# Kernel optimization log

Measured on AMD Instinct MI355X. Metric: run time of the kernel, lower is better.

The kernel has to match this reference:

```python
import jax, jax.numpy as jnp
import numpy as np

N_NODES = 100000
N_EDGES = 1600000
D = 64
N_LAYERS = 5  # hops=4 -> hops+1 GraphConv layers


def setup_inputs() -> dict:
    key = jax.random.key(0)
    k1, k2, k3, k4, k5, k6 = jax.random.split(key, 6)
    x = jax.random.normal(k1, (N_NODES, D), dtype=jnp.float32)
    edge_index = jax.random.randint(k2, (2, N_EDGES), 0, N_NODES, dtype=jnp.int64)
    edge_weight = jax.random.uniform(k3, (N_EDGES,), dtype=jnp.float32)
    # Per-layer params (all dims are 64 so we can stack): PyG GraphConv has
    # lin_rel (with bias) applied to the aggregated messages and lin_root
    # (no bias) applied to the node's own features.
    scale = 1.0 / np.sqrt(D)
    W_rel = jax.random.normal(k4, (N_LAYERS, D, D), dtype=jnp.float32) * scale
    b_rel = jnp.zeros((N_LAYERS, D), dtype=jnp.float32)
    W_root = jax.random.normal(k5, (N_LAYERS, D, D), dtype=jnp.float32) * scale
    return {"x": x, "edge_index": edge_index, "edge_weight": edge_weight,
            "W_rel": W_rel, "b_rel": b_rel, "W_root": W_root}


def _graph_conv(x, src, dst, edge_weight, W_rel_i, b_rel_i, W_root_i):
    # message: x_j * w_e ; aggregate: scatter-add onto destination nodes
    msg = x[src] * edge_weight[:, None]               # [E, D] gather
    agg = jax.ops.segment_sum(msg, dst, num_segments=N_NODES)  # [N, D] scatter
    return agg @ W_rel_i + b_rel_i + x @ W_root_i


def reference(x, edge_index, edge_weight, W_rel, b_rel, W_root):
    src, dst = edge_index[0], edge_index[1]
    h = x
    for i in range(N_LAYERS - 1):
        h = _graph_conv(h, src, dst, edge_weight, W_rel[i], b_rel[i], W_root[i])
        h = jax.nn.relu(h)
    h = _graph_conv(h, src, dst, edge_weight, W_rel[-1], b_rel[-1], W_root[-1])
    return h
```

## Files before the change

### kernel.cpp

```cpp
#include <hip/hip_runtime.h>

#define N_NODES 100000
#define N_EDGES 1600000
#define D 64
#define N_LAYERS 5
#define FB 1000
#define BN 100
#define NX 8
#define BCAP_X 320
#define BCAP 2048
#define BIN_BLOCKS 512
#define BIN_THREADS 512
#define BIN_CHUNK 3125

typedef unsigned short u16;
typedef unsigned long long u64;
typedef __attribute__((ext_vector_type(8))) short bf16x8;
typedef __attribute__((ext_vector_type(4))) float f32x4;

__device__ __forceinline__ float bf2f(u16 u) {
    union { unsigned int i; float f; } v;
    v.i = ((unsigned int)u) << 16;
    return v.f;
}
__device__ __forceinline__ u16 f2bf(float f) {
    union { float f; unsigned int i; } v;
    v.f = f;
    unsigned int r = v.i + 0x7FFFu + ((v.i >> 16) & 1u);
    return (u16)(r >> 16);
}
__device__ __forceinline__ float bf2f_lo(unsigned int pk) {
    union { unsigned int i; float f; } v;
    v.i = pk << 16;
    return v.f;
}
__device__ __forceinline__ float bf2f_hi(unsigned int pk) {
    union { unsigned int i; float f; } v;
    v.i = pk & 0xFFFF0000u;
    return v.f;
}


__global__ __launch_bounds__(1024) void initcur_kernel(int* __restrict__ fcur)
{
    int i = blockIdx.x * 1024 + threadIdx.x;
    if (i < NX * FB) fcur[i] = i * BCAP_X;
}

__global__ __launch_bounds__(BIN_THREADS) void bin_kernel(
    const int* __restrict__ src, const int* __restrict__ dst,
    const float* __restrict__ ew, int* __restrict__ fcur,
    u64* __restrict__ stag)
{
    __shared__ int hc[FB];
    const int xbase = (blockIdx.x & (NX - 1)) * FB;
    for (int b = threadIdx.x; b < FB; b += BIN_THREADS) hc[b] = 0;
    __syncthreads();
    const int e0 = blockIdx.x * BIN_CHUNK;
    for (int e = e0 + threadIdx.x; e < e0 + BIN_CHUNK; e += BIN_THREADS) {
        int d = dst[e];
        atomicAdd(&hc[d / BN], 1);
    }
    __syncthreads();
    for (int b = threadIdx.x; b < FB; b += BIN_THREADS) {
        int c = hc[b];
        if (c) hc[b] = atomicAdd(&fcur[xbase + b], c);
    }
    __syncthreads();
    for (int e = e0 + threadIdx.x; e < e0 + BIN_CHUNK; e += BIN_THREADS) {
        int d = dst[e];
        int b = d / BN;
        int pos = atomicAdd(&hc[b], 1);
        int s   = __builtin_nontemporal_load(&src[e]);
        float w = __builtin_nontemporal_load(&ew[e]);
        unsigned int pk = (unsigned int)((d - b * BN) << 17) | (unsigned int)s;
        u64 rec = ((u64)(unsigned int)__float_as_int(w) << 32) | pk;
        stag[pos] = rec;
    }
}

__global__ __launch_bounds__(1024) void fscan_kernel(
    const int* __restrict__ fcur, int* __restrict__ fbase,
    int* __restrict__ rowptr)
{
    __shared__ int s[1024];
    int t = threadIdx.x;
    int v = 0;
    if (t < FB) {
        #pragma unroll
        for (int x = 0; x < NX; ++x) {
            int cell = x * FB + t;
            v += fcur[cell] - cell * BCAP_X;
        }
    }
    s[t] = v;
    __syncthreads();
    for (int off = 1; off < 1024; off <<= 1) {
        int u = (t >= off) ? s[t - off] : 0;
        __syncthreads();
        s[t] += u;
        __syncthreads();
    }
    if (t < FB) fbase[t] = s[t] - v;
    if (t == FB - 1) {
        fbase[FB] = s[t];
        rowptr[N_NODES] = s[t];
    }
}

__global__ __launch_bounds__(256) void sort_kernel(
    const u64* __restrict__ stag, const int* __restrict__ fcur,
    const int* __restrict__ fbase, int* __restrict__ rowptr,
    int2* __restrict__ edges)
{
    __shared__ u64 ls[BCAP];
    __shared__ int cnt[BN];
    __shared__ int cur[BN];
    __shared__ int sc[128];
    const int b = blockIdx.x;
    const int base = fbase[b];
    const int t = threadIdx.x;
    for (int i = t; i < BN; i += 256) cnt[i] = 0;
    __syncthreads();
    int ofs = 0;
    #pragma unroll
    for (int x = 0; x < NX; ++x) {
        int cell = x * FB + b;
        int sz = fcur[cell] - cell * BCAP_X;
        const u64* sp = stag + (size_t)cell * BCAP_X;
        for (int i = t; i < sz; i += 256) {
            u64 r = __builtin_nontemporal_load(&sp[i]);
            ls[ofs + i] = r;
            atomicAdd(&cnt[((unsigned int)r) >> 17], 1);
        }
        ofs += sz;
    }
    const int size = ofs;
    __syncthreads();
    if (t < 128) sc[t] = (t < BN) ? cnt[t] : 0;
    __syncthreads();
    for (int off = 1; off < 128; off <<= 1) {
        int u = 0;
        if (t < 128 && t >= off) u = sc[t - off];
        __syncthreads();
        if (t < 128) sc[t] += u;
        __syncthreads();
    }
    if (t < BN) {
        int excl = sc[t] - cnt[t];
        rowptr[b * BN + t] = base + excl;
        cur[t] = excl;
    }
    __syncthreads();
    for (int i = t; i < size; i += 256) {
        u64 r = ls[i];
        unsigned int lo = (unsigned int)r;
        int dloc = lo >> 17;
        int rank = atomicAdd(&cur[dloc], 1);
        edges[base + rank] = make_int2((int)(lo & 0x1FFFFu),
                                       (int)(unsigned int)(r >> 32));
    }
}

__global__ __launch_bounds__(256) void f2bf_kernel(
    const float* __restrict__ in, u16* __restrict__ out)
{
    int i = blockIdx.x * 256 + threadIdx.x;
    if (i >= (N_NODES * D) / 4) return;
    float4 v = ((const float4*)in)[i];
    ushort4 o;
    o.x = f2bf(v.x); o.y = f2bf(v.y); o.z = f2bf(v.z); o.w = f2bf(v.w);
    ((ushort4*)out)[i] = o;
}

__global__ __launch_bounds__(256) void wprep_kernel(
    const float* __restrict__ Wrel, const float* __restrict__ Wroot,
    u16* __restrict__ W2T)
{
    int i = blockIdx.x * 256 + threadIdx.x;
    if (i >= N_LAYERS * 64 * 128) return;
    int l = i / (64 * 128);
    int rem = i % (64 * 128);
    int n = rem >> 7;
    int k = rem & 127;
    float v = (k < 64) ? Wrel[l * 4096 + k * 64 + n]
                       : Wroot[l * 4096 + (k - 64) * 64 + n];
    W2T[i] = f2bf(v);
}

__global__ __launch_bounds__(512) void layer_kernel(
    const u16* __restrict__ hin, const int* __restrict__ rowptr,
    const int2* __restrict__ edges, const u16* __restrict__ W2T,
    const float* __restrict__ brel,
    u16* __restrict__ hout_bf, float* __restrict__ hout_f32, int relu)
{
    __shared__ u16 aggs[16][64];
    const int wave = threadIdx.x >> 6;
    const int lane = threadIdx.x & 63;
    const int nb16 = blockIdx.x * 16;
    const int sl   = lane & 31;
    const int half = lane >> 5;

    {
        int nl = 2 * wave + half;
        int node = nb16 + nl;
        float acc0 = 0.f, acc1 = 0.f;
        int b = rowptr[node];
        int e = rowptr[node + 1];
        for (int base = b; base < e; base += 32) {
            int cnt = min(32, e - base);
            int idx = 0;
            float wv = 0.f;
            if (sl < cnt) {
                int2 p = edges[base + sl];
                idx = p.x;
                wv = __int_as_float(p.y);
            }
            int j = 0;
            for (; j + 8 <= cnt; j += 8) {
                int s0 = __shfl(idx, j + 0, 32), s1 = __shfl(idx, j + 1, 32);
                int s2 = __shfl(idx, j + 2, 32), s3 = __shfl(idx, j + 3, 32);
                int s4 = __shfl(idx, j + 4, 32), s5 = __shfl(idx, j + 5, 32);
                int s6 = __shfl(idx, j + 6, 32), s7 = __shfl(idx, j + 7, 32);
                float w0 = __shfl(wv, j + 0, 32), w1 = __shfl(wv, j + 1, 32);
                float w2 = __shfl(wv, j + 2, 32), w3 = __shfl(wv, j + 3, 32);
                float w4 = __shfl(wv, j + 4, 32), w5 = __shfl(wv, j + 5, 32);
                float w6 = __shfl(wv, j + 6, 32), w7 = __shfl(wv, j + 7, 32);
                unsigned int p0 = *(const unsigned int*)(hin + ((size_t)s0 << 6) + sl * 2);
                unsigned int p1 = *(const unsigned int*)(hin + ((size_t)s1 << 6) + sl * 2);
                unsigned int p2 = *(const unsigned int*)(hin + ((size_t)s2 << 6) + sl * 2);
                unsigned int p3 = *(const unsigned int*)(hin + ((size_t)s3 << 6) + sl * 2);
                unsigned int p4 = *(const unsigned int*)(hin + ((size_t)s4 << 6) + sl * 2);
                unsigned int p5 = *(const unsigned int*)(hin + ((size_t)s5 << 6) + sl * 2);
                unsigned int p6 = *(const unsigned int*)(hin + ((size_t)s6 << 6) + sl * 2);
                unsigned int p7 = *(const unsigned int*)(hin + ((size_t)s7 << 6) + sl * 2);
                acc0 += bf2f_lo(p0) * w0 + bf2f_lo(p1) * w1
                      + bf2f_lo(p2) * w2 + bf2f_lo(p3) * w3
                      + bf2f_lo(p4) * w4 + bf2f_lo(p5) * w5
                      + bf2f_lo(p6) * w6 + bf2f_lo(p7) * w7;
                acc1 += bf2f_hi(p0) * w0 + bf2f_hi(p1) * w1
                      + bf2f_hi(p2) * w2 + bf2f_hi(p3) * w3
                      + bf2f_hi(p4) * w4 + bf2f_hi(p5) * w5
                      + bf2f_hi(p6) * w6 + bf2f_hi(p7) * w7;
            }
            for (; j < cnt; ++j) {
                int s = __shfl(idx, j, 32);
                float w = __shfl(wv, j, 32);
                unsigned int pk = *(const unsigned int*)(hin + ((size_t)s << 6) + sl * 2);
                acc0 += bf2f_lo(pk) * w;
                acc1 += bf2f_hi(pk) * w;
            }
        }
        int u16idx = (nl << 6) | ((sl * 2) ^ ((nl & 7) << 3));
        unsigned int o = ((unsigned int)f2bf(acc1) << 16) | f2bf(acc0);
        *(unsigned int*)(&aggs[0][0] + u16idx) = o;
    }
    __syncthreads();

    if (wave < 4) {
        const int nt = wave;
        const int m = lane & 15;
        const int q = lane >> 4;

        bf16x8 a[4];
        {
            int r0 = (m << 6) | ((q * 8) ^ ((m & 7) << 3));
            int r1 = (m << 6) | ((32 + q * 8) ^ ((m & 7) << 3));
            a[0] = *(const bf16x8*)(&aggs[0][0] + r0);
            a[1] = *(const bf16x8*)(&aggs[0][0] + r1);
        }
        size_t rowa = (size_t)(nb16 + m) << 6;
        a[2] = *(const bf16x8*)(hin + rowa + q * 8);
        a[3] = *(const bf16x8*)(hin + rowa + 32 + q * 8);

        bf16x8 bfr[4];
        #pragma unroll
        for (int kk = 0; kk < 4; ++kk)
            bfr[kk] = *(const bf16x8*)(W2T + (size_t)(nt * 16 + m) * 128
                                       + kk * 32 + q * 8);

        float bv = brel[nt * 16 + m];
        f32x4 acc = (f32x4){bv, bv, bv, bv};
        #pragma unroll
        for (int kk = 0; kk < 4; ++kk)
            acc = __builtin_amdgcn_mfma_f32_16x16x32_bf16(a[kk], bfr[kk],
                                                          acc, 0, 0, 0);

        #pragma unroll
        for (int r = 0; r < 4; ++r) {
            int n2 = nb16 + q * 4 + r;
            float v = acc[r];
            if (relu) v = fmaxf(v, 0.f);
            int dim = nt * 16 + m;
            if (hout_f32) hout_f32[(size_t)n2 * 64 + dim] = v;
            else          hout_bf [(size_t)n2 * 64 + dim] = f2bf(v);
        }
    }
}

extern "C" void kernel_launch(void* const* d_in, const int* in_sizes, int n_in,
                              void* d_out, int out_size, void* d_ws, size_t ws_size,
                              hipStream_t stream)
{
    const float* x     = (const float*)d_in[0];
    const int*   ei    = (const int*)d_in[1];
    const float* ew    = (const float*)d_in[2];
    const float* Wrel  = (const float*)d_in[3];
    const float* brel  = (const float*)d_in[4];
    const float* Wroot = (const float*)d_in[5];
    float* out = (float*)d_out;

    const int* src = ei;
    const int* dst = ei + N_EDGES;

    const size_t featb_bytes = (size_t)N_NODES * D * 2;
    char* ws = (char*)d_ws;
    size_t off = 0;
    u16*  hb     = (u16*)(ws + off);  off += featb_bytes;
    u16*  hb2    = (u16*)(ws + off);  off += featb_bytes;
    u16*  W2T    = (u16*)(ws + off);  off += (size_t)N_LAYERS * 64 * 128 * 2;
    int*  rowptr = (int*)(ws + off);  off += 400016;
    int*  fcur   = (int*)(ws + off);  off += NX * FB * 4;
    int*  fbase  = (int*)(ws + off);  off += (FB + 1) * 4 + 60;
    int2* edges  = (int2*)(ws + off); off += (size_t)N_EDGES * 8;

    u64* stag = (u64*)ws;

    u16* hbuf[2] = {hb, hb2};

    const int cblocks = (N_NODES * D / 4 + 255) / 256;
    const int wblocks = (N_LAYERS * 64 * 128 + 255) / 256;
    const int lblocks = N_NODES / 16;

    initcur_kernel<<<8, 1024, 0, stream>>>(fcur);
    bin_kernel<<<BIN_BLOCKS, BIN_THREADS, 0, stream>>>(src, dst, ew, fcur, stag);
    fscan_kernel<<<1, 1024, 0, stream>>>(fcur, fbase, rowptr);
    sort_kernel<<<FB, 256, 0, stream>>>(stag, fcur, fbase, rowptr, edges);
    f2bf_kernel<<<cblocks, 256, 0, stream>>>(x, hb);
    wprep_kernel<<<wblocks, 256, 0, stream>>>(Wrel, Wroot, W2T);

    for (int layer = 0; layer < N_LAYERS; ++layer) {
        int last = (layer == N_LAYERS - 1);
        layer_kernel<<<lblocks, 512, 0, stream>>>(
            hbuf[layer & 1], rowptr, edges,
            W2T + (size_t)layer * 64 * 128,
            brel + (size_t)layer * D,
            last ? nullptr : hbuf[(layer + 1) & 1],
            last ? out : nullptr,
            last ? 0 : 1);
    }
}
```

Baseline: 397.2 us.

## Assign one wave per node with half-waves splitting edges, scalar edge loads

The gather phase changes from two nodes per wave (each half-wave handling one node) to one node per wave, with the two half-waves processing alternate edges and combining their partial sums through a cross-half shuffle. Edge records are now read as wave-uniform 64-bit loads with readfirstlane row bounds instead of being loaded per lane and broadcast via shuffles. Block size doubles to 1024 threads so each block still covers 16 nodes. This removes the shuffle broadcasts and balances per-node degree across a full wave, at the cost of twice as many threads, an extra reduction step, and lower occupancy headroom per block.

```diff
diff --git a/kernel.cpp b/kernel.cpp
--- a/kernel.cpp
+++ b/kernel.cpp
@@ -188,7 +188,7 @@
     W2T[i] = f2bf(v);
 }
 
-__global__ __launch_bounds__(512) void layer_kernel(
+__global__ __launch_bounds__(1024) void layer_kernel(
     const u16* __restrict__ hin, const int* __restrict__ rowptr,
     const int2* __restrict__ edges, const u16* __restrict__ W2T,
     const float* __restrict__ brel,
@@ -199,61 +199,56 @@
     const int lane = threadIdx.x & 63;
     const int nb16 = blockIdx.x * 16;
     const int sl   = lane & 31;
-    const int half = lane >> 5;
+    const int eo   = lane >> 5;
 
     {
-        int nl = 2 * wave + half;
-        int node = nb16 + nl;
+        const int node = nb16 + wave;
+        const int b = __builtin_amdgcn_readfirstlane(rowptr[node]);
+        const int e = __builtin_amdgcn_readfirstlane(rowptr[node + 1]);
+        const u64* eseg = (const u64*)edges;
         float acc0 = 0.f, acc1 = 0.f;
-        int b = rowptr[node];
-        int e = rowptr[node + 1];
-        for (int base = b; base < e; base += 32) {
-            int cnt = min(32, e - base);
-            int idx = 0;
-            float wv = 0.f;
-            if (sl < cnt) {
-                int2 p = edges[base + sl];
-                idx = p.x;
-                wv = __int_as_float(p.y);
+        int j = b;
+
+        #define PAIR(ra, rb) {                                               \
+            int   s_ = (int)(unsigned int)(eo ? (rb) : (ra));                \
+            float w_ = __int_as_float((int)(unsigned int)                    \
+                                      ((eo ? (rb) : (ra)) >> 32));           \
+            unsigned int p_ = *(const unsigned int*)                         \
+                              (hin + ((size_t)s_ << 6) + sl * 2);            \
+            acc0 += bf2f_lo(p_) * w_;                                        \
+            acc1 += bf2f_hi(p_) * w_; }
+
+        for (; j + 8 <= e; j += 8) {
+            u64 r0 = eseg[j + 0], r1 = eseg[j + 1];
+            u64 r2 = eseg[j + 2], r3 = eseg[j + 3];
+            u64 r4 = eseg[j + 4], r5 = eseg[j + 5];
+            u64 r6 = eseg[j + 6], r7 = eseg[j + 7];
+            PAIR(r0, r1); PAIR(r2, r3); PAIR(r4, r5); PAIR(r6, r7);
+        }
+        for (; j + 2 <= e; j += 2) {
+            u64 ra = eseg[j], rb = eseg[j + 1];
+            PAIR(ra, rb);
+        }
+        if (j < e) {
+            u64 ra = eseg[j];
+            if (eo == 0) {
+                int   s_ = (int)(unsigned int)ra;
+                float w_ = __int_as_float((int)(unsigned int)(ra >> 32));
+                unsigned int p_ = *(const unsigned int*)
+                                  (hin + ((size_t)s_ << 6) + sl * 2);
+                acc0 += bf2f_lo(p_) * w_;
+                acc1 += bf2f_hi(p_) * w_;
             }
-            int j = 0;
-            for (; j + 8 <= cnt; j += 8) {
-                int s0 = __shfl(idx, j + 0, 32), s1 = __shfl(idx, j + 1, 32);
-                int s2 = __shfl(idx, j + 2, 32), s3 = __shfl(idx, j + 3, 32);
-                int s4 = __shfl(idx, j + 4, 32), s5 = __shfl(idx, j + 5, 32);
-                int s6 = __shfl(idx, j + 6, 32), s7 = __shfl(idx, j + 7, 32);
-                float w0 = __shfl(wv, j + 0, 32), w1 = __shfl(wv, j + 1, 32);
-                float w2 = __shfl(wv, j + 2, 32), w3 = __shfl(wv, j + 3, 32);
-                float w4 = __shfl(wv, j + 4, 32), w5 = __shfl(wv, j + 5, 32);
-                float w6 = __shfl(wv, j + 6, 32), w7 = __shfl(wv, j + 7, 32);
-                unsigned int p0 = *(const unsigned int*)(hin + ((size_t)s0 << 6) + sl * 2);
-                unsigned int p1 = *(const unsigned int*)(hin + ((size_t)s1 << 6) + sl * 2);
-                unsigned int p2 = *(const unsigned int*)(hin + ((size_t)s2 << 6) + sl * 2);
-                unsigned int p3 = *(const unsigned int*)(hin + ((size_t)s3 << 6) + sl * 2);
-                unsigned int p4 = *(const unsigned int*)(hin + ((size_t)s4 << 6) + sl * 2);
-                unsigned int p5 = *(const unsigned int*)(hin + ((size_t)s5 << 6) + sl * 2);
-                unsigned int p6 = *(const unsigned int*)(hin + ((size_t)s6 << 6) + sl * 2);
-                unsigned int p7 = *(const unsigned int*)(hin + ((size_t)s7 << 6) + sl * 2);
-                acc0 += bf2f_lo(p0) * w0 + bf2f_lo(p1) * w1
-                      + bf2f_lo(p2) * w2 + bf2f_lo(p3) * w3
-                      + bf2f_lo(p4) * w4 + bf2f_lo(p5) * w5
-                      + bf2f_lo(p6) * w6 + bf2f_lo(p7) * w7;
-                acc1 += bf2f_hi(p0) * w0 + bf2f_hi(p1) * w1
-                      + bf2f_hi(p2) * w2 + bf2f_hi(p3) * w3
-                      + bf2f_hi(p4) * w4 + bf2f_hi(p5) * w5
-                      + bf2f_hi(p6) * w6 + bf2f_hi(p7) * w7;
-            }
-            for (; j < cnt; ++j) {
-                int s = __shfl(idx, j, 32);
-                float w = __shfl(wv, j, 32);
-                unsigned int pk = *(const unsigned int*)(hin + ((size_t)s << 6) + sl * 2);
-                acc0 += bf2f_lo(pk) * w;
-                acc1 += bf2f_hi(pk) * w;
-            }
-        }
-        int u16idx = (nl << 6) | ((sl * 2) ^ ((nl & 7) << 3));
-        unsigned int o = ((unsigned int)f2bf(acc1) << 16) | f2bf(acc0);
-        *(unsigned int*)(&aggs[0][0] + u16idx) = o;
+        }
+        #undef PAIR
+
+        acc0 += __shfl_xor(acc0, 32);
+        acc1 += __shfl_xor(acc1, 32);
+        if (eo == 0) {
+            int u16idx = (wave << 6) | ((sl * 2) ^ ((wave & 7) << 3));
+            unsigned int o = ((unsigned int)f2bf(acc1) << 16) | f2bf(acc0);
+            *(unsigned int*)(&aggs[0][0] + u16idx) = o;
+        }
     }
     __syncthreads();
 
@@ -341,7 +336,7 @@
 
     for (int layer = 0; layer < N_LAYERS; ++layer) {
         int last = (layer == N_LAYERS - 1);
-        layer_kernel<<<lblocks, 512, 0, stream>>>(
+        layer_kernel<<<lblocks, 1024, 0, stream>>>(
             hbuf[layer & 1], rowptr, edges,
             W2T + (size_t)layer * 64 * 128,
             brel + (size_t)layer * D,
```

Result: slower. 447.9 us (+12.8%).
